# Optimization experiments

Measured on AMD Instinct MI355X. Metric: run time of the kernel, lower is better.

## Reference

```python
import jax, jax.numpy as jnp
import numpy as np

NEG_SLOPE = 0.2
EPS = 1e-16

N_NODES = 50000
N_EDGES = 800000
N_QUERY = 100000


def setup_inputs() -> dict:
    key = jax.random.key(0)
    ks = jax.random.split(key, 12)
    x = jax.random.normal(ks[0], (N_NODES, 128), dtype=jnp.float32)
    edge_index = jax.random.randint(ks[1], (2, N_EDGES), 0, N_NODES, dtype=jnp.int64)
    edge_label_index = jax.random.randint(ks[2], (2, N_QUERY), 0, N_NODES, dtype=jnp.int64)
    # layer 1: in=128 -> out=256, heads=4, per-head dim 64
    W1 = jax.random.normal(ks[3], (128, 256), dtype=jnp.float32) * 0.08
    a1_src = jax.random.normal(ks[4], (4, 64), dtype=jnp.float32) * 0.08
    a1_dst = jax.random.normal(ks[5], (4, 64), dtype=jnp.float32) * 0.08
    b1 = jnp.zeros((256,), dtype=jnp.float32)
    # layer 2: in=256 -> out=32, heads=2, per-head dim 16
    W2 = jax.random.normal(ks[6], (256, 32), dtype=jnp.float32) * 0.08
    a2_src = jax.random.normal(ks[7], (2, 16), dtype=jnp.float32) * 0.08
    a2_dst = jax.random.normal(ks[8], (2, 16), dtype=jnp.float32) * 0.08
    b2 = jnp.zeros((32,), dtype=jnp.float32)
    return {"x": x, "edge_index": edge_index, "edge_label_index": edge_label_index,
            "W1": W1, "a1_src": a1_src, "a1_dst": a1_dst, "b1": b1,
            "W2": W2, "a2_src": a2_src, "a2_dst": a2_dst, "b2": b2}


def gat_layer(x, src, dst, W, a_src, a_dst, b, heads):
    """Multi-head GAT: gather -> edge logits -> segment softmax over dst -> scatter-add."""
    n = x.shape[0]
    out = W.shape[1]
    c = out // heads
    h = (x @ W).reshape(n, heads, c)                       # [N,H,C]
    # per-node attention contributions: [N,H]
    alpha_s = jnp.einsum('nhc,hc->nh', h, a_src)
    alpha_d = jnp.einsum('nhc,hc->nh', h, a_dst)
    e = alpha_s[src] + alpha_d[dst]                         # [E,H]
    e = jax.nn.leaky_relu(e, NEG_SLOPE)
    # segment softmax over incoming edges of each dst node
    m = jax.ops.segment_max(e, dst, num_segments=n)         # [N,H]
    m = jnp.where(jnp.isfinite(m), m, 0.0)
    ex = jnp.exp(e - m[dst])                                # [E,H]
    s = jax.ops.segment_sum(ex, dst, num_segments=n)        # [N,H]
    w = ex / (s[dst] + EPS)                                 # [E,H]
    msg = h[src] * w[:, :, None]                            # [E,H,C]
    agg = jax.ops.segment_sum(msg, dst, num_segments=n)     # [N,H,C]
    return agg.reshape(n, out) + b


def reference(x, edge_index, edge_label_index, W1, a1_src, a1_dst, b1, W2, a2_src, a2_dst, b2):
    n = x.shape[0]
    loops = jnp.arange(n, dtype=edge_index.dtype)
    src = jnp.concatenate([edge_index[0], loops])
    dst = jnp.concatenate([edge_index[1], loops])
    # encode (dropout p=0 and use_bn=False are identities)
    z = gat_layer(x, src, dst, W1, a1_src, a1_dst, b1, heads=4)
    z = jax.nn.relu(z)
    z = gat_layer(z, src, dst, W2, a2_src, a2_dst, b2, heads=2)
    # decode: dot product of endpoint embeddings
    return (z[edge_label_index[0]] * z[edge_label_index[1]]).sum(axis=-1)
```

## Files before the change

### kernel.cpp

```cpp
#include <hip/hip_runtime.h>

#define NEG_SLOPE 0.2f
#define EPSV 1e-16f

__device__ __forceinline__ float lrelu(float e){ return (e > 0.f) ? e : NEG_SLOPE*e; }

__global__ void k_deg(const int* __restrict__ ei, int E, int N, int* __restrict__ deg){
  int t = blockIdx.x*blockDim.x + threadIdx.x;
  int ET = E + N;
  if (t >= ET) return;
  int dst = (t < E) ? ei[E + t] : (t - E);
  atomicAdd(&deg[dst], 1);
}

__global__ void k_scan(const int* __restrict__ deg, int N, int* __restrict__ rs){
  __shared__ int sums[1024];
  int tid = threadIdx.x;
  int chunk = (N + 1023) >> 10;
  int s = tid*chunk, e = min(s+chunk, N);
  int sum = 0;
  for (int i = s; i < e; ++i) sum += deg[i];
  sums[tid] = sum;
  __syncthreads();
  for (int off = 1; off < 1024; off <<= 1){
    int v = (tid >= off) ? sums[tid-off] : 0;
    __syncthreads();
    sums[tid] += v;
    __syncthreads();
  }
  int run = (tid == 0) ? 0 : sums[tid-1];
  for (int i = s; i < e; ++i){ rs[i] = run; run += deg[i]; }
  if (tid == 1023) rs[N] = run;
}

__global__ void k_fill(const int* __restrict__ ei, int E, int N,
                       const int* __restrict__ rs, int* __restrict__ cnt,
                       int* __restrict__ csr_s){
  int t = blockIdx.x*blockDim.x + threadIdx.x;
  int ET = E + N;
  if (t >= ET) return;
  int src, dst;
  if (t < E){ src = ei[t]; dst = ei[E + t]; } else { src = dst = t - E; }
  int pos = atomicAdd(&cnt[dst], 1);
  csr_s[rs[dst] + pos] = src;
}

__global__ __launch_bounds__(256) void k_gemm1(const float* __restrict__ x, const float* __restrict__ W1,
                                               const float* __restrict__ a1s, const float* __restrict__ a1d,
                                               int N, float* __restrict__ h1,
                                               float* __restrict__ als, float* __restrict__ ald){
  __shared__ float xs[8][128];
  int bn = blockIdx.x * 8;
  int tid = threadIdx.x;
  {
    int m = tid >> 5, k4 = tid & 31;
    int node = bn + m;
    float4 v = (node < N) ? ((const float4*)x)[(size_t)node*32 + k4]
                          : make_float4(0.f,0.f,0.f,0.f);
    ((float4*)xs[m])[k4] = v;
  }
  __syncthreads();
  float acc[8];
  #pragma unroll
  for (int m = 0; m < 8; ++m) acc[m] = 0.f;
  int j = tid;
  for (int k = 0; k < 128; ++k){
    float w = W1[k*256 + j];
    #pragma unroll
    for (int m = 0; m < 8; ++m) acc[m] = fmaf(xs[m][k], w, acc[m]);
  }
  int head = j >> 6;
  int lane = j & 63;
  float cas = a1s[head*64 + lane];
  float cad = a1d[head*64 + lane];
  #pragma unroll
  for (int m = 0; m < 8; ++m){
    int node = bn + m;
    if (node < N) h1[(size_t)node*256 + j] = acc[m];
    float vs = acc[m]*cas, vd = acc[m]*cad;
    #pragma unroll
    for (int o = 32; o; o >>= 1){ vs += __shfl_xor(vs, o, 64); vd += __shfl_xor(vd, o, 64); }
    if (lane == 0 && node < N){ als[node*4+head] = vs; ald[node*4+head] = vd; }
  }
}

__global__ __launch_bounds__(256) void k_gemm2(const float* __restrict__ z1, const float* __restrict__ W2,
                                               const float* __restrict__ a2s, const float* __restrict__ a2d,
                                               int N, float* __restrict__ h2,
                                               float* __restrict__ als, float* __restrict__ ald){
  __shared__ float zs[8][256];
  int bn = blockIdx.x * 8;
  int tid = threadIdx.x;
  {
    int m = tid >> 6, k4 = tid & 63;
    int node = bn + m;
    const float4 zero = make_float4(0.f,0.f,0.f,0.f);
    ((float4*)zs[m])[k4]      = (node < N)   ? ((const float4*)z1)[(size_t)node*64 + k4] : zero;
    int m2 = m + 4, node2 = bn + m2;
    ((float4*)zs[m2])[k4]     = (node2 < N)  ? ((const float4*)z1)[(size_t)node2*64 + k4] : zero;
  }
  __syncthreads();
  int j = tid & 31;
  int m = tid >> 5;
  float acc = 0.f;
  for (int k = 0; k < 256; ++k) acc = fmaf(zs[m][k], W2[k*32 + j], acc);
  int node = bn + m;
  int head = j >> 4, lane = j & 15;
  if (node < N) h2[(size_t)node*32 + j] = acc;
  float vs = acc * a2s[head*16 + lane];
  float vd = acc * a2d[head*16 + lane];
  #pragma unroll
  for (int o = 8; o; o >>= 1){ vs += __shfl_xor(vs, o, 64); vd += __shfl_xor(vd, o, 64); }
  if (lane == 0 && node < N){ als[node*2+head] = vs; ald[node*2+head] = vd; }
}

__global__ __launch_bounds__(256) void k_agg1(const int* __restrict__ rs, const int* __restrict__ csr_s,
                                              const float* __restrict__ als, const float* __restrict__ ald,
                                              const float* __restrict__ h1, const float* __restrict__ b1,
                                              int N, float* __restrict__ z1){
  __shared__ int    sidx[256];
  __shared__ float  sexp[256*4];
  __shared__ float4 accl[4][64];
  __shared__ float  sl[4][64];
  int node = blockIdx.x;
  int tid = threadIdx.x;
  int w = tid >> 6, lane = tid & 63;
  int head = lane >> 4;
  int beg = rs[node], end = rs[node+1];
  float4 acc = make_float4(0.f,0.f,0.f,0.f);
  float s = 0.f;
  for (int base = beg; base < end; base += 256){
    int cnt = min(256, end - base);
    if (tid < cnt) sidx[tid] = csr_s[base + tid];
    __syncthreads();
    for (int t = tid; t < cnt*4; t += 256){
      int e = t >> 2, h = t & 3;
      int sv = sidx[e];
      sexp[t] = __expf(lrelu(als[sv*4 + h] + ald[node*4 + h]));
    }
    __syncthreads();
    int e = w;
    for (; e + 12 < cnt; e += 16){
      int s0 = sidx[e], s1 = sidx[e+4], s2 = sidx[e+8], s3 = sidx[e+12];
      float x0 = sexp[e*4+head], x1 = sexp[(e+4)*4+head];
      float x2 = sexp[(e+8)*4+head], x3 = sexp[(e+12)*4+head];
      float4 v0 = ((const float4*)h1)[(size_t)s0*64 + lane];
      float4 v1 = ((const float4*)h1)[(size_t)s1*64 + lane];
      float4 v2 = ((const float4*)h1)[(size_t)s2*64 + lane];
      float4 v3 = ((const float4*)h1)[(size_t)s3*64 + lane];
      acc.x = fmaf(v0.x, x0, acc.x); acc.y = fmaf(v0.y, x0, acc.y);
      acc.z = fmaf(v0.z, x0, acc.z); acc.w = fmaf(v0.w, x0, acc.w);
      acc.x = fmaf(v1.x, x1, acc.x); acc.y = fmaf(v1.y, x1, acc.y);
      acc.z = fmaf(v1.z, x1, acc.z); acc.w = fmaf(v1.w, x1, acc.w);
      acc.x = fmaf(v2.x, x2, acc.x); acc.y = fmaf(v2.y, x2, acc.y);
      acc.z = fmaf(v2.z, x2, acc.z); acc.w = fmaf(v2.w, x2, acc.w);
      acc.x = fmaf(v3.x, x3, acc.x); acc.y = fmaf(v3.y, x3, acc.y);
      acc.z = fmaf(v3.z, x3, acc.z); acc.w = fmaf(v3.w, x3, acc.w);
      s += (x0 + x1) + (x2 + x3);
    }
    for (; e < cnt; e += 4){
      int s0 = sidx[e];
      float x0 = sexp[e*4+head];
      float4 v0 = ((const float4*)h1)[(size_t)s0*64 + lane];
      acc.x = fmaf(v0.x, x0, acc.x); acc.y = fmaf(v0.y, x0, acc.y);
      acc.z = fmaf(v0.z, x0, acc.z); acc.w = fmaf(v0.w, x0, acc.w);
      s += x0;
    }
    __syncthreads();
  }
  accl[w][lane] = acc;
  sl[w][lane] = s;
  __syncthreads();
  if (tid < 64){
    float4 a0 = accl[0][tid], a1 = accl[1][tid], a2 = accl[2][tid], a3 = accl[3][tid];
    float st = sl[0][tid] + sl[1][tid] + sl[2][tid] + sl[3][tid];
    float inv = 1.0f / (st + EPSV);
    float4 bb = ((const float4*)b1)[tid];
    float4 r;
    r.x = fmaf(a0.x + a1.x + a2.x + a3.x, inv, bb.x);
    r.y = fmaf(a0.y + a1.y + a2.y + a3.y, inv, bb.y);
    r.z = fmaf(a0.z + a1.z + a2.z + a3.z, inv, bb.z);
    r.w = fmaf(a0.w + a1.w + a2.w + a3.w, inv, bb.w);
    r.x = fmaxf(r.x, 0.f); r.y = fmaxf(r.y, 0.f);
    r.z = fmaxf(r.z, 0.f); r.w = fmaxf(r.w, 0.f);
    ((float4*)z1)[(size_t)node*64 + tid] = r;
  }
}

__global__ __launch_bounds__(256) void k_agg2(const int* __restrict__ rs, const int* __restrict__ csr_s,
                                              const float* __restrict__ als, const float* __restrict__ ald,
                                              const float* __restrict__ h2, const float* __restrict__ b2,
                                              int N, float* __restrict__ z2){
  int tid = threadIdx.x;
  int node = blockIdx.x*4 + (tid >> 6);
  if (node >= N) return;
  int lane = tid & 63;
  int slot = lane >> 3;
  int q    = lane & 7;
  int head = q >> 2;
  float aldn = ald[node*2 + head];
  int beg = rs[node], end = rs[node+1];
  float4 acc = make_float4(0.f,0.f,0.f,0.f);
  float s = 0.f;
  for (int i = beg + slot; i < end; i += 8){
    int s0 = csr_s[i];
    float x0 = __expf(lrelu(als[s0*2+head] + aldn));
    float4 v0 = ((const float4*)h2)[(size_t)s0*8 + q];
    acc.x = fmaf(v0.x, x0, acc.x); acc.y = fmaf(v0.y, x0, acc.y);
    acc.z = fmaf(v0.z, x0, acc.z); acc.w = fmaf(v0.w, x0, acc.w);
    s += x0;
  }
  #pragma unroll
  for (int o = 8; o < 64; o <<= 1){
    acc.x += __shfl_xor(acc.x, o, 64); acc.y += __shfl_xor(acc.y, o, 64);
    acc.z += __shfl_xor(acc.z, o, 64); acc.w += __shfl_xor(acc.w, o, 64);
    s += __shfl_xor(s, o, 64);
  }
  if (slot == 0){
    float inv = 1.0f / (s + EPSV);
    float4 bb = ((const float4*)b2)[q];
    float4 r;
    r.x = fmaf(acc.x, inv, bb.x); r.y = fmaf(acc.y, inv, bb.y);
    r.z = fmaf(acc.z, inv, bb.z); r.w = fmaf(acc.w, inv, bb.w);
    ((float4*)z2)[(size_t)node*8 + q] = r;
  }
}

__global__ void k_decode(const int* __restrict__ eli, int NQ,
                         const float* __restrict__ z2, float* __restrict__ out){
  int t = blockIdx.x*blockDim.x + threadIdx.x;
  if (t >= NQ*8) return;
  int qq = t >> 3, q = t & 7;
  int a = eli[qq], b = eli[NQ + qq];
  float4 va = ((const float4*)z2)[(size_t)a*8 + q];
  float4 vb = ((const float4*)z2)[(size_t)b*8 + q];
  float p = va.x*vb.x + va.y*vb.y + va.z*vb.z + va.w*vb.w;
  p += __shfl_xor(p, 1, 64); p += __shfl_xor(p, 2, 64); p += __shfl_xor(p, 4, 64);
  if (q == 0) out[qq] = p;
}

extern "C" void kernel_launch(void* const* d_in, const int* in_sizes, int n_in,
                              void* d_out, int out_size, void* d_ws, size_t ws_size,
                              hipStream_t stream) {
  const float* x   = (const float*)d_in[0];
  const int*   ei  = (const int*)d_in[1];
  const int*   eli = (const int*)d_in[2];
  const float* W1  = (const float*)d_in[3];
  const float* a1s = (const float*)d_in[4];
  const float* a1d = (const float*)d_in[5];
  const float* b1  = (const float*)d_in[6];
  const float* W2  = (const float*)d_in[7];
  const float* a2s = (const float*)d_in[8];
  const float* a2d = (const float*)d_in[9];
  const float* b2  = (const float*)d_in[10];
  float* out = (float*)d_out;

  int N  = in_sizes[0] / 128;
  int E  = in_sizes[1] / 2;
  int NQ = in_sizes[2] / 2;
  int ET = E + N;

  char* base = (char*)d_ws;
  size_t off = 0;
  auto alloc = [&](size_t elems)->char*{ char* r = base + off; off += elems*4; return r; };
  int*   deg   = (int*)  alloc(N);
  int*   cnt   = (int*)  alloc(N);
  size_t zbytes = off;
  int*   rs    = (int*)  alloc(N+1);
  int*   csr_s = (int*)  alloc(ET);
  float* al1s  = (float*)alloc((size_t)N*4);
  float* al1d  = (float*)alloc((size_t)N*4);
  float* al2s  = (float*)alloc((size_t)N*2);
  float* al2d  = (float*)alloc((size_t)N*2);
  float* h1    = (float*)alloc((size_t)N*256);
  float* z1    = (float*)alloc((size_t)N*256);
  float* h2    = (float*)alloc((size_t)N*32);
  float* z2    = (float*)alloc((size_t)N*32);
  (void)ws_size; (void)n_in; (void)out_size;

  hipMemsetAsync(d_ws, 0, zbytes, stream);

  k_deg <<<(ET+255)/256, 256, 0, stream>>>(ei, E, N, deg);
  k_scan<<<1, 1024, 0, stream>>>(deg, N, rs);
  k_fill<<<(ET+255)/256, 256, 0, stream>>>(ei, E, N, rs, cnt, csr_s);

  k_gemm1<<<(N+7)/8, 256, 0, stream>>>(x, W1, a1s, a1d, N, h1, al1s, al1d);
  k_agg1<<<N, 256, 0, stream>>>(rs, csr_s, al1s, al1d, h1, b1, N, z1);

  k_gemm2<<<(N+7)/8, 256, 0, stream>>>(z1, W2, a2s, a2d, N, h2, al2s, al2d);
  k_agg2<<<(N+3)/4, 256, 0, stream>>>(rs, csr_s, al2s, al2d, h2, b2, N, z2);

  k_decode<<<((long long)NQ*8+255)/256, 256, 0, stream>>>(eli, NQ, z2, out);
}
```

Measured before the change: 547.1 us.

## Fuse CSR build into cooperative kernel and store layer-1 features as bf16

Replaces the memset, degree, single-block scan and fill kernels with one cooperative grid kernel. It does the zeroing, degree count, multi-block scan and fill in phases separated by grid syncs. Layer-1 projected features are stored as bf16 and widened during aggregation, which halves the gather traffic in the dominant aggregation kernel. The bf16 storage adds rounding error. The cooperative launch of 1024 blocks assumes all blocks can be resident at once and adds grid-sync cost.

```diff
diff --git a/kernel.cpp b/kernel.cpp
--- a/kernel.cpp
+++ b/kernel.cpp
@@ -1,53 +1,82 @@
 #include <hip/hip_runtime.h>
+#include <hip/hip_cooperative_groups.h>
+
+namespace cg = cooperative_groups;
 
 #define NEG_SLOPE 0.2f
 #define EPSV 1e-16f
 
 __device__ __forceinline__ float lrelu(float e){ return (e > 0.f) ? e : NEG_SLOPE*e; }
-
-__global__ void k_deg(const int* __restrict__ ei, int E, int N, int* __restrict__ deg){
-  int t = blockIdx.x*blockDim.x + threadIdx.x;
+__device__ __forceinline__ float bf2f(unsigned short u){ return __uint_as_float((unsigned)u << 16); }
+__device__ __forceinline__ unsigned short f2bf(float f){
+  unsigned u = __float_as_uint(f);
+  u += 0x7FFFu + ((u >> 16) & 1u);
+  return (unsigned short)(u >> 16);
+}
+
+__global__ void k_csr(const int* __restrict__ ei, int E, int N,
+                      int* __restrict__ deg, int* __restrict__ cnt,
+                      int* __restrict__ rs, int* __restrict__ csr_s,
+                      int* __restrict__ bsum){
+  cg::grid_group grid = cg::this_grid();
+  const int nb = gridDim.x;
+  int tid = threadIdx.x, bid = blockIdx.x;
+  int gt = bid*blockDim.x + tid, gs = nb*blockDim.x;
   int ET = E + N;
-  if (t >= ET) return;
-  int dst = (t < E) ? ei[E + t] : (t - E);
-  atomicAdd(&deg[dst], 1);
-}
-
-__global__ void k_scan(const int* __restrict__ deg, int N, int* __restrict__ rs){
-  __shared__ int sums[1024];
-  int tid = threadIdx.x;
-  int chunk = (N + 1023) >> 10;
-  int s = tid*chunk, e = min(s+chunk, N);
-  int sum = 0;
-  for (int i = s; i < e; ++i) sum += deg[i];
-  sums[tid] = sum;
-  __syncthreads();
-  for (int off = 1; off < 1024; off <<= 1){
-    int v = (tid >= off) ? sums[tid-off] : 0;
-    __syncthreads();
-    sums[tid] += v;
-    __syncthreads();
-  }
-  int run = (tid == 0) ? 0 : sums[tid-1];
-  for (int i = s; i < e; ++i){ rs[i] = run; run += deg[i]; }
-  if (tid == 1023) rs[N] = run;
-}
-
-__global__ void k_fill(const int* __restrict__ ei, int E, int N,
-                       const int* __restrict__ rs, int* __restrict__ cnt,
-                       int* __restrict__ csr_s){
-  int t = blockIdx.x*blockDim.x + threadIdx.x;
-  int ET = E + N;
-  if (t >= ET) return;
-  int src, dst;
-  if (t < E){ src = ei[t]; dst = ei[E + t]; } else { src = dst = t - E; }
-  int pos = atomicAdd(&cnt[dst], 1);
-  csr_s[rs[dst] + pos] = src;
+  __shared__ int red[256];
+  __shared__ int sc[1024];
+  __shared__ int ts[256];
+
+  for (int i = gt; i < N; i += gs){ deg[i] = 0; cnt[i] = 0; }
+  grid.sync();
+  for (int t = gt; t < ET; t += gs){
+    int dst = (t < E) ? ei[E + t] : (t - E);
+    atomicAdd(&deg[dst], 1);
+  }
+  grid.sync();
+  int chunk = (N + nb - 1) / nb;
+  int s0 = bid*chunk, e0 = min(s0 + chunk, N);
+  {
+    int sum = 0;
+    for (int i = s0 + tid; i < e0; i += 256) sum += deg[i];
+    red[tid] = sum; __syncthreads();
+    for (int o = 128; o; o >>= 1){ if (tid < o) red[tid] += red[tid+o]; __syncthreads(); }
+    if (tid == 0) bsum[bid] = red[0];
+  }
+  grid.sync();
+  if (bid == 0){
+    for (int i = tid; i < 1024; i += 256) sc[i] = (i < nb) ? bsum[i] : 0;
+    __syncthreads();
+    int a0 = sc[4*tid], a1 = sc[4*tid+1], a2 = sc[4*tid+2], a3 = sc[4*tid+3];
+    int l1 = a0+a1, l2 = l1+a2, l3 = l2+a3;
+    ts[tid] = l3; __syncthreads();
+    for (int o = 1; o < 256; o <<= 1){
+      int v = (tid >= o) ? ts[tid-o] : 0; __syncthreads();
+      ts[tid] += v; __syncthreads();
+    }
+    int excl = (tid == 0) ? 0 : ts[tid-1];
+    sc[4*tid] = excl; sc[4*tid+1] = excl+a0; sc[4*tid+2] = excl+l1; sc[4*tid+3] = excl+l2;
+    __syncthreads();
+    for (int i = tid; i < nb; i += 256) bsum[i] = sc[i];
+  }
+  grid.sync();
+  if (tid == 0){
+    int r = bsum[bid];
+    for (int i = s0; i < e0; ++i){ rs[i] = r; r += deg[i]; }
+    if (e0 == N) rs[N] = r;
+  }
+  grid.sync();
+  for (int t = gt; t < ET; t += gs){
+    int src, dst;
+    if (t < E){ src = ei[t]; dst = ei[E + t]; } else { src = dst = t - E; }
+    int pos = atomicAdd(&cnt[dst], 1);
+    csr_s[rs[dst] + pos] = src;
+  }
 }
 
 __global__ __launch_bounds__(256) void k_gemm1(const float* __restrict__ x, const float* __restrict__ W1,
                                                const float* __restrict__ a1s, const float* __restrict__ a1d,
-                                               int N, float* __restrict__ h1,
+                                               int N, unsigned short* __restrict__ h1b,
                                                float* __restrict__ als, float* __restrict__ ald){
   __shared__ float xs[8][128];
   int bn = blockIdx.x * 8;
@@ -76,7 +105,7 @@
   #pragma unroll
   for (int m = 0; m < 8; ++m){
     int node = bn + m;
-    if (node < N) h1[(size_t)node*256 + j] = acc[m];
+    if (node < N) h1b[(size_t)node*256 + j] = f2bf(acc[m]);
     float vs = acc[m]*cas, vd = acc[m]*cad;
     #pragma unroll
     for (int o = 32; o; o >>= 1){ vs += __shfl_xor(vs, o, 64); vd += __shfl_xor(vd, o, 64); }
@@ -116,7 +145,7 @@
 
 __global__ __launch_bounds__(256) void k_agg1(const int* __restrict__ rs, const int* __restrict__ csr_s,
                                               const float* __restrict__ als, const float* __restrict__ ald,
-                                              const float* __restrict__ h1, const float* __restrict__ b1,
+                                              const unsigned short* __restrict__ h1b, const float* __restrict__ b1,
                                               int N, float* __restrict__ z1){
   __shared__ int    sidx[256];
   __shared__ float  sexp[256*4];
@@ -127,6 +156,7 @@
   int w = tid >> 6, lane = tid & 63;
   int head = lane >> 4;
   int beg = rs[node], end = rs[node+1];
+  const ushort4* h1v = (const ushort4*)h1b;
   float4 acc = make_float4(0.f,0.f,0.f,0.f);
   float s = 0.f;
   for (int base = beg; base < end; base += 256){
@@ -144,26 +174,26 @@
       int s0 = sidx[e], s1 = sidx[e+4], s2 = sidx[e+8], s3 = sidx[e+12];
       float x0 = sexp[e*4+head], x1 = sexp[(e+4)*4+head];
       float x2 = sexp[(e+8)*4+head], x3 = sexp[(e+12)*4+head];
-      float4 v0 = ((const float4*)h1)[(size_t)s0*64 + lane];
-      float4 v1 = ((const float4*)h1)[(size_t)s1*64 + lane];
-      float4 v2 = ((const float4*)h1)[(size_t)s2*64 + lane];
-      float4 v3 = ((const float4*)h1)[(size_t)s3*64 + lane];
-      acc.x = fmaf(v0.x, x0, acc.x); acc.y = fmaf(v0.y, x0, acc.y);
-      acc.z = fmaf(v0.z, x0, acc.z); acc.w = fmaf(v0.w, x0, acc.w);
-      acc.x = fmaf(v1.x, x1, acc.x); acc.y = fmaf(v1.y, x1, acc.y);
-      acc.z = fmaf(v1.z, x1, acc.z); acc.w = fmaf(v1.w, x1, acc.w);
-      acc.x = fmaf(v2.x, x2, acc.x); acc.y = fmaf(v2.y, x2, acc.y);
-      acc.z = fmaf(v2.z, x2, acc.z); acc.w = fmaf(v2.w, x2, acc.w);
-      acc.x = fmaf(v3.x, x3, acc.x); acc.y = fmaf(v3.y, x3, acc.y);
-      acc.z = fmaf(v3.z, x3, acc.z); acc.w = fmaf(v3.w, x3, acc.w);
+      ushort4 u0 = h1v[(size_t)s0*64 + lane];
+      ushort4 u1 = h1v[(size_t)s1*64 + lane];
+      ushort4 u2 = h1v[(size_t)s2*64 + lane];
+      ushort4 u3 = h1v[(size_t)s3*64 + lane];
+      acc.x = fmaf(bf2f(u0.x), x0, acc.x); acc.y = fmaf(bf2f(u0.y), x0, acc.y);
+      acc.z = fmaf(bf2f(u0.z), x0, acc.z); acc.w = fmaf(bf2f(u0.w), x0, acc.w);
+      acc.x = fmaf(bf2f(u1.x), x1, acc.x); acc.y = fmaf(bf2f(u1.y), x1, acc.y);
+      acc.z = fmaf(bf2f(u1.z), x1, acc.z); acc.w = fmaf(bf2f(u1.w), x1, acc.w);
+      acc.x = fmaf(bf2f(u2.x), x2, acc.x); acc.y = fmaf(bf2f(u2.y), x2, acc.y);
+      acc.z = fmaf(bf2f(u2.z), x2, acc.z); acc.w = fmaf(bf2f(u2.w), x2, acc.w);
+      acc.x = fmaf(bf2f(u3.x), x3, acc.x); acc.y = fmaf(bf2f(u3.y), x3, acc.y);
+      acc.z = fmaf(bf2f(u3.z), x3, acc.z); acc.w = fmaf(bf2f(u3.w), x3, acc.w);
       s += (x0 + x1) + (x2 + x3);
     }
     for (; e < cnt; e += 4){
       int s0 = sidx[e];
       float x0 = sexp[e*4+head];
-      float4 v0 = ((const float4*)h1)[(size_t)s0*64 + lane];
-      acc.x = fmaf(v0.x, x0, acc.x); acc.y = fmaf(v0.y, x0, acc.y);
-      acc.z = fmaf(v0.z, x0, acc.z); acc.w = fmaf(v0.w, x0, acc.w);
+      ushort4 u0 = h1v[(size_t)s0*64 + lane];
+      acc.x = fmaf(bf2f(u0.x), x0, acc.x); acc.y = fmaf(bf2f(u0.y), x0, acc.y);
+      acc.z = fmaf(bf2f(u0.z), x0, acc.z); acc.w = fmaf(bf2f(u0.w), x0, acc.w);
       s += x0;
     }
     __syncthreads();
@@ -265,27 +295,27 @@
   auto alloc = [&](size_t elems)->char*{ char* r = base + off; off += elems*4; return r; };
   int*   deg   = (int*)  alloc(N);
   int*   cnt   = (int*)  alloc(N);
-  size_t zbytes = off;
+  int*   bsum  = (int*)  alloc(1024);
   int*   rs    = (int*)  alloc(N+1);
   int*   csr_s = (int*)  alloc(ET);
   float* al1s  = (float*)alloc((size_t)N*4);
   float* al1d  = (float*)alloc((size_t)N*4);
   float* al2s  = (float*)alloc((size_t)N*2);
   float* al2d  = (float*)alloc((size_t)N*2);
-  float* h1    = (float*)alloc((size_t)N*256);
+  unsigned short* h1b = (unsigned short*)alloc((size_t)N*128);
   float* z1    = (float*)alloc((size_t)N*256);
   float* h2    = (float*)alloc((size_t)N*32);
   float* z2    = (float*)alloc((size_t)N*32);
   (void)ws_size; (void)n_in; (void)out_size;
 
-  hipMemsetAsync(d_ws, 0, zbytes, stream);
-
-  k_deg <<<(ET+255)/256, 256, 0, stream>>>(ei, E, N, deg);
-  k_scan<<<1, 1024, 0, stream>>>(deg, N, rs);
-  k_fill<<<(ET+255)/256, 256, 0, stream>>>(ei, E, N, rs, cnt, csr_s);
-
-  k_gemm1<<<(N+7)/8, 256, 0, stream>>>(x, W1, a1s, a1d, N, h1, al1s, al1d);
-  k_agg1<<<N, 256, 0, stream>>>(rs, csr_s, al1s, al1d, h1, b1, N, z1);
+  {
+    void* args[] = {(void*)&ei, (void*)&E, (void*)&N, (void*)&deg, (void*)&cnt,
+                    (void*)&rs, (void*)&csr_s, (void*)&bsum};
+    hipLaunchCooperativeKernel((void*)k_csr, dim3(1024), dim3(256), args, 0, stream);
+  }
+
+  k_gemm1<<<(N+7)/8, 256, 0, stream>>>(x, W1, a1s, a1d, N, h1b, al1s, al1d);
+  k_agg1<<<N, 256, 0, stream>>>(rs, csr_s, al1s, al1d, h1b, b1, N, z1);
 
   k_gemm2<<<(N+7)/8, 256, 0, stream>>>(z1, W2, a2s, a2d, N, h2, al2s, al2d);
   k_agg2<<<(N+3)/4, 256, 0, stream>>>(rs, csr_s, al2s, al2d, h2, b2, N, z2);
```

New measurement: 913.3 us. 66.9% more time.
